# Performance work log

Hardware: AMD Instinct MI355X
Metric: run time of the kernel (lower is better)

## Reference

```python
import jax, jax.numpy as jnp
import numpy as np

N, C, H, W = 4, 128, 64, 64


def setup_inputs() -> dict:
    key = jax.random.key(0)
    ks = jax.random.split(key, 4)
    s = 1.0 / np.sqrt(C).astype(np.float32)  # conv2d default-init scale
    return {
        "x": jax.random.normal(ks[0], (N, C, H, W), dtype=jnp.float32),
        "Wq": jax.random.normal(ks[1], (C, C), dtype=jnp.float32) * s,
        "bq": jnp.zeros((C,), dtype=jnp.float32),
        "Wk": jax.random.normal(ks[2], (C, C), dtype=jnp.float32) * s,
        "bk": jnp.zeros((C,), dtype=jnp.float32),
        "Wv": jax.random.normal(ks[3], (C, C), dtype=jnp.float32) * s,
        "bv": jnp.zeros((C,), dtype=jnp.float32),
    }


def reference(x, Wq, bq, Wk, bk, Wv, bv):
    n, c, h, w = x.shape
    xf = x.reshape(n, c, h * w)  # [N, C, L], L = H*W
    # 1x1 convs == per-pixel channel mixing
    q = jnp.einsum('oc,ncl->nol', Wq, xf) + bq[:, None]
    k = jnp.einsum('oc,ncl->nol', Wk, xf) + bk[:, None]
    v = jnp.einsum('oc,ncl->nol', Wv, xf) + bv[:, None]
    # scores[l, m] = sum_c k[c,l] * q[c,m]  (matmul(k^T, q))
    scale = jnp.asarray(1.0 / np.sqrt(c), x.dtype)
    scores = jnp.einsum('ncl,ncm->nlm', k, q) * scale  # [N, L, L]
    temp = jax.nn.softmax(scores, axis=-1)
    attn = jnp.einsum('ncl,nlm->ncm', v, temp)  # [N, C, L]
    return x + attn.reshape(n, c, h, w)
```

## Files before the change

### kernel.cpp

```cpp
#include <hip/hip_runtime.h>
#include <hip/hip_bf16.h>
#include <stdint.h>

#define NB 4
#define CH 128
#define LL 4096

typedef __attribute__((ext_vector_type(8))) short short8;
typedef __attribute__((ext_vector_type(4))) short short4b;
typedef __attribute__((ext_vector_type(4))) float floatx4;
typedef __attribute__((ext_vector_type(16))) float floatx16;


static __device__ __forceinline__ short f2bf(float f) {
    uint32_t u = __float_as_uint(f);
    u += 0x7fffu + ((u >> 16) & 1u);
    return (short)(u >> 16);
}

__global__ __launch_bounds__(256) void wprep_kernel(
    const float* __restrict__ Wq, const float* __restrict__ Wk,
    const float* __restrict__ Wv, short* __restrict__ Wf)
{
    const int g = blockIdx.x * 256 + threadIdx.x;
    const int mat = g >> 14;
    const int rem = g & 16383;
    const int o   = rem >> 7;
    const int c   = rem & 127;
    const float* W = (mat == 0) ? Wq : (mat == 1) ? Wk : Wv;
    float v = W[o * CH + c];
    if (mat == 1) v *= 0.08838834764831845f;
    Wf[(size_t)mat * 16384 + (o >> 4) * 2048 + (c >> 5) * 512
       + ((c >> 3) & 3) * 128 + (o & 15) * 8 + (c & 7)] = f2bf(v);
}

__global__ __launch_bounds__(256) void proj_kernel(
    const float* __restrict__ x, const short* __restrict__ Wf,
    const float* __restrict__ bq, const float* __restrict__ bk,
    const float* __restrict__ bv,
    short* __restrict__ Qf, short* __restrict__ Kf, short* __restrict__ Vp)
{
    const int b    = blockIdx.x;
    const int n    = b >> 7;
    const int lt   = b & 127;
    const int l0   = lt << 5;
    const int tid  = threadIdx.x;
    const int wave = tid >> 6;
    const int lane = tid & 63;
    const int quad = lane >> 4;
    const int mc   = lane & 15;

    __shared__ short Xb[32][136];

    {
        const int sl = tid & 31;
        const int cg = tid >> 5;
        const float* xp = x + ((size_t)n * CH + cg * 16) * LL + l0 + sl;
        short8 buf;
        #pragma unroll
        for (int i = 0; i < 16; ++i) {
            buf[i & 7] = f2bf(xp[(size_t)i * LL]);
            if ((i & 7) == 7)
                *(short8*)(void*)&Xb[sl][cg * 16 + (i & 8)] = buf;
        }
    }
    __syncthreads();

    const int lt2 = wave >> 1;
    const int oh  = wave & 1;
    const int gt  = lt * 2 + lt2;

    short8 xf[4];
    #pragma unroll
    for (int s = 0; s < 4; ++s)
        xf[s] = *(const short8*)(const void*)&Xb[lt2 * 16 + mc][32 * s + quad * 8];

    const size_t obase = ((size_t)n * 256 + gt) * 2048;

    #pragma unroll
    for (int mat = 0; mat < 3; ++mat) {
        const short* Wm = Wf + (size_t)mat * 16384;
        const float* bb = (mat == 0) ? bq : (mat == 1) ? bk : bv;
        const float bscale = (mat == 1) ? 0.08838834764831845f : 1.0f;
        #pragma unroll
        for (int ot = oh * 4; ot < oh * 4 + 4; ++ot) {
            floatx4 acc = {0.f, 0.f, 0.f, 0.f};
            #pragma unroll
            for (int s = 0; s < 4; ++s)
                acc = __builtin_amdgcn_mfma_f32_16x16x32_bf16(
                    *(const short8*)(const void*)(Wm + ot * 2048 + s * 512 + lane * 8),
                    xf[s], acc, 0, 0, 0);
            const int c0 = ot * 16 + 4 * quad;
            if (mat < 2) {
                short4b pv;
                #pragma unroll
                for (int r = 0; r < 4; ++r)
                    pv[r] = f2bf(acc[r] + bb[c0 + r] * bscale);
                short* dst = ((mat == 0) ? Qf : Kf) + obase
                           + (c0 >> 5) * 512 + ((c0 >> 3) & 3) * 128
                           + mc * 8 + (c0 & 7);
                *(short4b*)(void*)dst = pv;
            } else {
                #pragma unroll
                for (int r = 0; r < 4; ++r)
                    Vp[obase + (c0 + r) * 16 + mc] = f2bf(acc[r] + bb[c0 + r]);
            }
        }
    }
}

__global__ __launch_bounds__(256, 4) void rowsum_kernel(
    const short* __restrict__ Qf, const short* __restrict__ Kf,
    float* __restrict__ Dsum)
{
    const int b    = blockIdx.x;
    const int n    = b >> 8;
    const int lt   = b & 255;
    const int wave = threadIdx.x >> 6;
    const int lane = threadIdx.x & 63;
    const int quad = lane >> 4;
    const int mc   = lane & 15;

    const short* Kb = Kf + ((size_t)n * 256 + lt) * 2048 + lane * 8;
    short8 kf[4];
    #pragma unroll
    for (int s = 0; s < 4; ++s) kf[s] = *(const short8*)(const void*)(Kb + s * 512);

    const short* Qn = Qf + (size_t)n * 524288 + (size_t)wave * 64 * 2048 + lane * 8;
    float rs[4] = {0.f, 0.f, 0.f, 0.f};

    for (int i = 0; i < 64; i += 4) {
        floatx4 a[4];
        #pragma unroll
        for (int j = 0; j < 4; ++j) a[j] = (floatx4){0.f, 0.f, 0.f, 0.f};
        #pragma unroll
        for (int s = 0; s < 4; ++s)
            #pragma unroll
            for (int j = 0; j < 4; ++j)
                a[j] = __builtin_amdgcn_mfma_f32_16x16x32_bf16(
                    kf[s],
                    *(const short8*)(const void*)(Qn + (size_t)(i + j) * 2048 + s * 512),
                    a[j], 0, 0, 0);
        #pragma unroll
        for (int j = 0; j < 4; ++j)
            #pragma unroll
            for (int r = 0; r < 4; ++r) rs[r] += __expf(a[j][r]);
    }

    #pragma unroll
    for (int r = 0; r < 4; ++r) {
        float v = rs[r];
        v += __shfl_xor(v, 1);
        v += __shfl_xor(v, 2);
        v += __shfl_xor(v, 4);
        v += __shfl_xor(v, 8);
        rs[r] = v;
    }
    if (mc == 0) {
        #pragma unroll
        for (int r = 0; r < 4; ++r)
            atomicAdd(&Dsum[(size_t)n * LL + lt * 16 + quad * 4 + r], rs[r]);
    }
}

__global__ __launch_bounds__(512, 4) void attn_out_kernel(
    const short* __restrict__ Qf, const short* __restrict__ Kf,
    const short* __restrict__ Vp, const float* __restrict__ Dsum,
    const float* __restrict__ x, float* __restrict__ out)
{
    const int b    = blockIdx.x;
    const int n    = b >> 7;
    const int m0   = (b & 127) << 5;
    const int tid  = threadIdx.x;
    const int wave = tid >> 6;
    const int lane = tid & 63;
    const int quad = lane >> 4;
    const int mc   = lane & 15;
    const int l32  = lane & 31;
    const int h    = lane >> 5;
    const int ct   = wave & 3;
    const int kh   = wave >> 2;

    __shared__ short P[2][32][136];
    __shared__ float Rbuf[4][64][16];

    const short* Qn  = Qf + (size_t)n * 524288;
    const short* Kn  = Kf + (size_t)n * 524288;
    const short* Vpn = Vp + (size_t)n * 524288;
    const float* Dn  = Dsum + (size_t)n * LL;

    short8 qf[2][4];
    #pragma unroll
    for (int mst = 0; mst < 2; ++mst)
        #pragma unroll
        for (int s = 0; s < 4; ++s)
            qf[mst][s] = *(const short8*)(const void*)(
                Qn + (size_t)((m0 >> 4) + mst) * 2048 + s * 512 + lane * 8);

    floatx16 acc;
    #pragma unroll
    for (int r = 0; r < 16; ++r) acc[r] = 0.f;

    for (int step = 0; step < 32; ++step) {
        const int lb = step << 7;
        const int p  = step & 1;

        short8 kfr[4];
        #pragma unroll
        for (int s = 0; s < 4; ++s)
            kfr[s] = *(const short8*)(const void*)(
                Kn + (size_t)(step * 8 + wave) * 2048 + s * 512 + lane * 8);
        const floatx4 ds = *(const floatx4*)(const void*)(Dn + lb + 16 * wave + quad * 4);
        float d[4];
        #pragma unroll
        for (int r = 0; r < 4; ++r) d[r] = 1.0f / ds[r];

        #pragma unroll
        for (int mst = 0; mst < 2; ++mst) {
            floatx4 sa = {0.f, 0.f, 0.f, 0.f};
            #pragma unroll
            for (int s = 0; s < 4; ++s)
                sa = __builtin_amdgcn_mfma_f32_16x16x32_bf16(kfr[s], qf[mst][s], sa, 0, 0, 0);
            short4b pv;
            #pragma unroll
            for (int r = 0; r < 4; ++r) pv[r] = f2bf(__expf(sa[r]) * d[r]);
            *(short4b*)(void*)&P[p][16 * mst + mc][16 * wave + quad * 4] = pv;
        }
        __syncthreads();

        #pragma unroll
        for (int i = 0; i < 4; ++i) {
            const int kc = kh * 4 + i;
            const short8 vf = *(const short8*)(const void*)(
                Vpn + (size_t)((lb >> 4) + kc) * 2048 + (32 * ct + l32) * 16 + 8 * h);
            const short8 pf = *(const short8*)(const void*)&P[p][l32][16 * kc + 8 * h];
            acc = __builtin_amdgcn_mfma_f32_32x32x16_bf16(vf, pf, acc, 0, 0, 0);
        }
    }

    __syncthreads();
    if (kh == 1)
        *(floatx16*)(void*)&Rbuf[ct][lane][0] = acc;
    __syncthreads();
    if (kh == 0) {
        const floatx16 o = *(const floatx16*)(const void*)&Rbuf[ct][lane][0];
        #pragma unroll
        for (int r = 0; r < 16; ++r) {
            const int c = 32 * ct + (r & 3) + 8 * (r >> 2) + 4 * h;
            const int m = m0 + l32;
            const size_t idx = ((size_t)n * CH + c) * LL + m;
            out[idx] = x[idx] + acc[r] + o[r];
        }
    }
}

extern "C" void kernel_launch(void* const* d_in, const int* in_sizes, int n_in,
                              void* d_out, int out_size, void* d_ws, size_t ws_size,
                              hipStream_t stream) {
    (void)in_sizes; (void)n_in; (void)out_size; (void)ws_size;
    const float* x  = (const float*)d_in[0];
    const float* Wq = (const float*)d_in[1];
    const float* bq = (const float*)d_in[2];
    const float* Wk = (const float*)d_in[3];
    const float* bk = (const float*)d_in[4];
    const float* Wv = (const float*)d_in[5];
    const float* bv = (const float*)d_in[6];
    float* out = (float*)d_out;

    char* ws = (char*)d_ws;
    short* Qf = (short*)(ws);
    short* Kf = (short*)(ws + 4194304);
    short* Vp = (short*)(ws + 8388608);
    float* Ds = (float*)(ws + 12582912);
    short* Wf = (short*)(ws + 12582912 + 65536);

    hipMemsetAsync(Ds, 0, 65536, stream);
    wprep_kernel<<<192, 256, 0, stream>>>(Wq, Wk, Wv, Wf);
    proj_kernel<<<512, 256, 0, stream>>>(x, Wf, bq, bk, bv, Qf, Kf, Vp);
    rowsum_kernel<<<1024, 256, 0, stream>>>(Qf, Kf, Ds);
    attn_out_kernel<<<512, 512, 0, stream>>>(Qf, Kf, Vp, Ds, x, out);
}
```

Measured before the change: 184.1 us.

## Enlarge tiles in rowsum and attention-output kernels for more operand reuse

The rowsum kernel now handles two K row-tiles per block, so each loaded Q fragment feeds twice as many MFMAs, and the grid is halved. The attention-output kernel moves to 1024-thread blocks covering 64 query columns and 256 keys per step, with 16 waves split over channel tile, query half and key half. This halves how often K and V are re-read per query column. In exchange Q fragments are reloaded from memory inside the step loop instead of being held in registers, occupancy drops to fewer, larger blocks with more shared memory, and only 256 blocks are launched.

```diff
diff --git a/kernel.cpp b/kernel.cpp
--- a/kernel.cpp
+++ b/kernel.cpp
@@ -109,68 +109,80 @@
     }
 }
 
-__global__ __launch_bounds__(256, 4) void rowsum_kernel(
+__global__ __launch_bounds__(256) void rowsum_kernel(
     const short* __restrict__ Qf, const short* __restrict__ Kf,
     float* __restrict__ Dsum)
 {
     const int b    = blockIdx.x;
-    const int n    = b >> 8;
-    const int lt   = b & 255;
+    const int n    = b >> 7;
+    const int tp   = b & 127;
     const int wave = threadIdx.x >> 6;
     const int lane = threadIdx.x & 63;
     const int quad = lane >> 4;
     const int mc   = lane & 15;
 
-    const short* Kb = Kf + ((size_t)n * 256 + lt) * 2048 + lane * 8;
-    short8 kf[4];
-    #pragma unroll
-    for (int s = 0; s < 4; ++s) kf[s] = *(const short8*)(const void*)(Kb + s * 512);
+    const short* Kb = Kf + ((size_t)n * 256 + tp * 2) * 2048 + lane * 8;
+    short8 kf[2][4];
+    #pragma unroll
+    for (int t = 0; t < 2; ++t)
+        #pragma unroll
+        for (int s = 0; s < 4; ++s)
+            kf[t][s] = *(const short8*)(const void*)(Kb + t * 2048 + s * 512);
 
     const short* Qn = Qf + (size_t)n * 524288 + (size_t)wave * 64 * 2048 + lane * 8;
-    float rs[4] = {0.f, 0.f, 0.f, 0.f};
-
-    for (int i = 0; i < 64; i += 4) {
-        floatx4 a[4];
-        #pragma unroll
-        for (int j = 0; j < 4; ++j) a[j] = (floatx4){0.f, 0.f, 0.f, 0.f};
-        #pragma unroll
-        for (int s = 0; s < 4; ++s)
-            #pragma unroll
-            for (int j = 0; j < 4; ++j)
-                a[j] = __builtin_amdgcn_mfma_f32_16x16x32_bf16(
-                    kf[s],
-                    *(const short8*)(const void*)(Qn + (size_t)(i + j) * 2048 + s * 512),
-                    a[j], 0, 0, 0);
-        #pragma unroll
-        for (int j = 0; j < 4; ++j)
-            #pragma unroll
-            for (int r = 0; r < 4; ++r) rs[r] += __expf(a[j][r]);
-    }
-
-    #pragma unroll
-    for (int r = 0; r < 4; ++r) {
-        float v = rs[r];
-        v += __shfl_xor(v, 1);
-        v += __shfl_xor(v, 2);
-        v += __shfl_xor(v, 4);
-        v += __shfl_xor(v, 8);
-        rs[r] = v;
-    }
-    if (mc == 0) {
-        #pragma unroll
-        for (int r = 0; r < 4; ++r)
-            atomicAdd(&Dsum[(size_t)n * LL + lt * 16 + quad * 4 + r], rs[r]);
-    }
-}
-
-__global__ __launch_bounds__(512, 4) void attn_out_kernel(
+    float rs[2][4] = {{0.f,0.f,0.f,0.f},{0.f,0.f,0.f,0.f}};
+
+    for (int i = 0; i < 64; i += 2) {
+        floatx4 a[2][2];
+        #pragma unroll
+        for (int t = 0; t < 2; ++t)
+            #pragma unroll
+            for (int j = 0; j < 2; ++j) a[t][j] = (floatx4){0.f,0.f,0.f,0.f};
+        #pragma unroll
+        for (int s = 0; s < 4; ++s) {
+            const short8 q0 = *(const short8*)(const void*)(Qn + (size_t)i * 2048 + s * 512);
+            const short8 q1 = *(const short8*)(const void*)(Qn + (size_t)(i + 1) * 2048 + s * 512);
+            #pragma unroll
+            for (int t = 0; t < 2; ++t) {
+                a[t][0] = __builtin_amdgcn_mfma_f32_16x16x32_bf16(kf[t][s], q0, a[t][0], 0, 0, 0);
+                a[t][1] = __builtin_amdgcn_mfma_f32_16x16x32_bf16(kf[t][s], q1, a[t][1], 0, 0, 0);
+            }
+        }
+        #pragma unroll
+        for (int t = 0; t < 2; ++t)
+            #pragma unroll
+            for (int j = 0; j < 2; ++j)
+                #pragma unroll
+                for (int r = 0; r < 4; ++r) rs[t][r] += __expf(a[t][j][r]);
+    }
+
+    #pragma unroll
+    for (int t = 0; t < 2; ++t) {
+        #pragma unroll
+        for (int r = 0; r < 4; ++r) {
+            float v = rs[t][r];
+            v += __shfl_xor(v, 1);
+            v += __shfl_xor(v, 2);
+            v += __shfl_xor(v, 4);
+            v += __shfl_xor(v, 8);
+            rs[t][r] = v;
+        }
+        if (mc == 0) {
+            #pragma unroll
+            for (int r = 0; r < 4; ++r)
+                atomicAdd(&Dsum[(size_t)n * LL + (tp * 2 + t) * 16 + quad * 4 + r], rs[t][r]);
+        }
+    }
+}
+
+__global__ __launch_bounds__(1024) void attn_out_kernel(
     const short* __restrict__ Qf, const short* __restrict__ Kf,
     const short* __restrict__ Vp, const float* __restrict__ Dsum,
     const float* __restrict__ x, float* __restrict__ out)
 {
     const int b    = blockIdx.x;
-    const int n    = b >> 7;
-    const int m0   = (b & 127) << 5;
+    const int n    = b >> 6;
+    const int m0   = (b & 63) << 6;
     const int tid  = threadIdx.x;
     const int wave = tid >> 6;
     const int lane = tid & 63;
@@ -179,48 +191,44 @@
     const int l32  = lane & 31;
     const int h    = lane >> 5;
     const int ct   = wave & 3;
-    const int kh   = wave >> 2;
-
-    __shared__ short P[2][32][136];
-    __shared__ float Rbuf[4][64][16];
+    const int mh   = (wave >> 2) & 1;
+    const int kh   = wave >> 3;
+
+    __shared__ short P[2][64][264];
+    __shared__ float Rbuf[4][2][64][16];
 
     const short* Qn  = Qf + (size_t)n * 524288;
     const short* Kn  = Kf + (size_t)n * 524288;
     const short* Vpn = Vp + (size_t)n * 524288;
     const float* Dn  = Dsum + (size_t)n * LL;
 
-    short8 qf[2][4];
-    #pragma unroll
-    for (int mst = 0; mst < 2; ++mst)
-        #pragma unroll
-        for (int s = 0; s < 4; ++s)
-            qf[mst][s] = *(const short8*)(const void*)(
-                Qn + (size_t)((m0 >> 4) + mst) * 2048 + s * 512 + lane * 8);
-
     floatx16 acc;
     #pragma unroll
     for (int r = 0; r < 16; ++r) acc[r] = 0.f;
 
-    for (int step = 0; step < 32; ++step) {
-        const int lb = step << 7;
+    for (int step = 0; step < 16; ++step) {
+        const int lb = step << 8;
         const int p  = step & 1;
 
         short8 kfr[4];
         #pragma unroll
         for (int s = 0; s < 4; ++s)
             kfr[s] = *(const short8*)(const void*)(
-                Kn + (size_t)(step * 8 + wave) * 2048 + s * 512 + lane * 8);
+                Kn + (size_t)(step * 16 + wave) * 2048 + s * 512 + lane * 8);
         const floatx4 ds = *(const floatx4*)(const void*)(Dn + lb + 16 * wave + quad * 4);
         float d[4];
         #pragma unroll
         for (int r = 0; r < 4; ++r) d[r] = 1.0f / ds[r];
 
         #pragma unroll
-        for (int mst = 0; mst < 2; ++mst) {
+        for (int mst = 0; mst < 4; ++mst) {
             floatx4 sa = {0.f, 0.f, 0.f, 0.f};
             #pragma unroll
-            for (int s = 0; s < 4; ++s)
-                sa = __builtin_amdgcn_mfma_f32_16x16x32_bf16(kfr[s], qf[mst][s], sa, 0, 0, 0);
+            for (int s = 0; s < 4; ++s) {
+                const short8 qfr = *(const short8*)(const void*)(
+                    Qn + (size_t)((m0 >> 4) + mst) * 2048 + s * 512 + lane * 8);
+                sa = __builtin_amdgcn_mfma_f32_16x16x32_bf16(kfr[s], qfr, sa, 0, 0, 0);
+            }
             short4b pv;
             #pragma unroll
             for (int r = 0; r < 4; ++r) pv[r] = f2bf(__expf(sa[r]) * d[r]);
@@ -229,25 +237,25 @@
         __syncthreads();
 
         #pragma unroll
-        for (int i = 0; i < 4; ++i) {
-            const int kc = kh * 4 + i;
+        for (int i = 0; i < 8; ++i) {
+            const int kc = kh * 8 + i;
             const short8 vf = *(const short8*)(const void*)(
                 Vpn + (size_t)((lb >> 4) + kc) * 2048 + (32 * ct + l32) * 16 + 8 * h);
-            const short8 pf = *(const short8*)(const void*)&P[p][l32][16 * kc + 8 * h];
+            const short8 pf = *(const short8*)(const void*)&P[p][32 * mh + l32][16 * kc + 8 * h];
             acc = __builtin_amdgcn_mfma_f32_32x32x16_bf16(vf, pf, acc, 0, 0, 0);
         }
     }
 
     __syncthreads();
     if (kh == 1)
-        *(floatx16*)(void*)&Rbuf[ct][lane][0] = acc;
+        *(floatx16*)(void*)&Rbuf[ct][mh][lane][0] = acc;
     __syncthreads();
     if (kh == 0) {
-        const floatx16 o = *(const floatx16*)(const void*)&Rbuf[ct][lane][0];
+        const floatx16 o = *(const floatx16*)(const void*)&Rbuf[ct][mh][lane][0];
         #pragma unroll
         for (int r = 0; r < 16; ++r) {
             const int c = 32 * ct + (r & 3) + 8 * (r >> 2) + 4 * h;
-            const int m = m0 + l32;
+            const int m = m0 + 32 * mh + l32;
             const size_t idx = ((size_t)n * CH + c) * LL + m;
             out[idx] = x[idx] + acc[r] + o[r];
         }
@@ -277,6 +285,6 @@
     hipMemsetAsync(Ds, 0, 65536, stream);
     wprep_kernel<<<192, 256, 0, stream>>>(Wq, Wk, Wv, Wf);
     proj_kernel<<<512, 256, 0, stream>>>(x, Wf, bq, bk, bv, Qf, Kf, Vp);
-    rowsum_kernel<<<1024, 256, 0, stream>>>(Qf, Kf, Ds);
-    attn_out_kernel<<<512, 512, 0, stream>>>(Qf, Kf, Vp, Ds, x, out);
-}
+    rowsum_kernel<<<512, 256, 0, stream>>>(Qf, Kf, Ds);
+    attn_out_kernel<<<256, 1024, 0, stream>>>(Qf, Kf, Vp, Ds, x, out);
+}
```

New measurement: 176.1 us. -4.3%, faster.
